# Kernel tuning notes

Measured on AMD Instinct MI355X. Metric: run time of the kernel, lower is better.

Reference implementation:

```python
import jax, jax.numpy as jnp
import numpy as np

N_NODES = 200000
N_EDGES = 800000
N_MOL = 10000
IN_DIM, HDIM, EDGE_DIM = 40, 64, 16
BN_EPS = 1e-5


def _bn_eval(h, gamma, beta, mean, var):
    # BatchNorm1d in eval mode (running stats)
    return gamma * (h - mean) * jax.lax.rsqrt(var + BN_EPS) + beta


def _gine(x, src, dst, edge_attr, We, be, W, b, gamma, beta, mean, var):
    # GINEConv (eps=0): agg_i = sum_{(j->i)} relu(x_j + lin_e(e_ji)); h = nn(x + agg)
    msg = jax.nn.relu(x[src] + edge_attr @ We.T + be)          # [E, d]
    agg = jax.ops.segment_sum(msg, dst, num_segments=x.shape[0])
    h = (x + agg) @ W.T + b                                    # Linear
    h = _bn_eval(h, gamma, beta, mean, var)                    # BatchNorm1d
    return jax.nn.leaky_relu(h)                                # LeakyReLU(0.01); Dropout is identity in eval


def setup_inputs() -> dict:
    key = jax.random.key(0)
    ks = jax.random.split(key, 40)
    d = {}
    d['x'] = jax.random.normal(ks[0], (N_NODES, IN_DIM), jnp.float32)
    d['edge_index'] = jax.random.randint(ks[1], (2, N_EDGES), 0, N_NODES, jnp.int32)
    d['edge_attr'] = jax.random.normal(ks[2], (N_EDGES, EDGE_DIM), jnp.float32)
    d['batch'] = jnp.sort(jax.random.randint(ks[3], (N_NODES,), 0, N_MOL, jnp.int32))
    i = 4
    def nrm(shape, scale=0.05):
        nonlocal i
        i += 1
        return jax.random.normal(ks[i - 1], shape, jnp.float32) * scale
    for l, din in ((1, IN_DIM), (2, HDIM), (3, HDIM)):
        d[f'We{l}'] = nrm((din, EDGE_DIM)); d[f'be{l}'] = nrm((din,))
        d[f'W{l}'] = nrm((HDIM, din)); d[f'b{l}'] = nrm((HDIM,))
        d[f'g{l}'] = jnp.ones((HDIM,), jnp.float32); d[f'bb{l}'] = jnp.zeros((HDIM,), jnp.float32)
        d[f'm{l}'] = nrm((HDIM,)); d[f'v{l}'] = jax.random.uniform(ks[i], (HDIM,), jnp.float32, 0.5, 1.5); i += 1
    D4 = 4 * HDIM
    d['Wl1'] = nrm((D4, D4)); d['bl1'] = nrm((D4,))
    d['Wl2'] = nrm((1, D4)); d['bl2'] = nrm((1,))
    return d


def reference(x, edge_index, edge_attr, batch,
              We1, be1, W1, b1, g1, bb1, m1, v1,
              We2, be2, W2, b2, g2, bb2, m2, v2,
              We3, be3, W3, b3, g3, bb3, m3, v3,
              Wl1, bl1, Wl2, bl2):
    src, dst = edge_index[0], edge_index[1]
    h1 = _gine(x, src, dst, edge_attr, We1, be1, W1, b1, g1, bb1, m1, v1)
    h2 = _gine(h1, src, dst, edge_attr, We2, be2, W2, b2, g2, bb2, m2, v2)
    h3 = _gine(h2, src, dst, edge_attr, We3, be3, W3, b3, g3, bb3, m3, v3)
    h_pool = jax.ops.segment_sum(h3, batch, num_segments=N_MOL)   # global_add_pool
    h_pool_ = h_pool[batch]                                       # repeat_interleave by per-mol counts
    h = jnp.concatenate([h1, h2, h3, h_pool_], axis=1)            # [N, 4*hdim]
    h = jax.nn.leaky_relu(h @ Wl1.T + bl1)
    return h @ Wl2.T + bl2                                        # [N, 1]
```

## Files before the change

kernel.cpp:

```cpp
#include <hip/hip_runtime.h>
#include <hip/hip_bf16.h>

#define N_NODES 200000
#define N_EDGES 800000
#define N_MOL   10000
#define HDIM    64
#define EDGE_DIM 16
#define BN_EPS 1e-5f
#define SCAN_BLOCKS ((N_NODES + 255) / 256)

typedef __attribute__((ext_vector_type(8))) short short8;
typedef __attribute__((ext_vector_type(4))) float f32x4;

__device__ __forceinline__ unsigned int pk2(float a, float b) {
    __hip_bfloat162 h = __float22bfloat162_rn(make_float2(a, b));
    union { __hip_bfloat162 h; unsigned int u; } c;
    c.h = h;
    return c.u;
}
__device__ __forceinline__ short8 cvt8(float4 a, float4 b) {
    union { short8 s; unsigned int u[4]; } r;
    r.u[0] = pk2(a.x, a.y); r.u[1] = pk2(a.z, a.w);
    r.u[2] = pk2(b.x, b.y); r.u[3] = pk2(b.z, b.w);
    return r.s;
}
__device__ __forceinline__ float bf2f(unsigned short u) {
    return __uint_as_float(((unsigned int)u) << 16);
}
__device__ __forceinline__ unsigned short f2bf(float a) {
    union { __hip_bfloat16 h; unsigned short u; } c;
    c.h = __float2bfloat16(a);
    return c.u;
}
__device__ __forceinline__ float4 bf4f(ushort4 u) {
    return make_float4(bf2f(u.x), bf2f(u.y), bf2f(u.z), bf2f(u.w));
}

__global__ __launch_bounds__(256) void cvtx_kernel(
    const float* __restrict__ x, unsigned short* __restrict__ xb)
{
    int i = blockIdx.x * 256 + threadIdx.x;
    if ((size_t)i * 4 >= (size_t)N_NODES * 40) return;
    float4 v = *(const float4*)(x + (size_t)i * 4);
    union { ushort4 s; unsigned int u[2]; } r;
    r.u[0] = pk2(v.x, v.y); r.u[1] = pk2(v.z, v.w);
    *(ushort4*)(xb + (size_t)i * 4) = r.s;
}

__global__ __launch_bounds__(256) void hist_kernel(
    const int* __restrict__ ei, int* __restrict__ counts)
{
    int e = blockIdx.x * 256 + threadIdx.x;
    if (e < N_EDGES) atomicAdd(&counts[ei[N_EDGES + e]], 1);
}

__global__ __launch_bounds__(256) void scan_phase_a(
    const int* __restrict__ counts,
    int* __restrict__ row_ptr, int* __restrict__ block_sums)
{
    __shared__ int lds[256];
    int t = threadIdx.x;
    int i = blockIdx.x * 256 + t;
    int v = (i < N_NODES) ? counts[i] : 0;
    lds[t] = v;
    __syncthreads();
    for (int off = 1; off < 256; off <<= 1) {
        int u = (t >= off) ? lds[t - off] : 0;
        __syncthreads();
        lds[t] += u;
        __syncthreads();
    }
    if (i < N_NODES) row_ptr[i] = lds[t] - v;
    if (t == 255) block_sums[blockIdx.x] = lds[255];
}

__global__ __launch_bounds__(1024) void scan_phase_b(
    int* __restrict__ block_sums)
{
    __shared__ int lds[1024];
    int t = threadIdx.x;
    int v = (t < SCAN_BLOCKS) ? block_sums[t] : 0;
    lds[t] = v;
    __syncthreads();
    for (int off = 1; off < 1024; off <<= 1) {
        int u = (t >= off) ? lds[t - off] : 0;
        __syncthreads();
        lds[t] += u;
        __syncthreads();
    }
    if (t < SCAN_BLOCKS) block_sums[t] = lds[t] - v;
}

__global__ __launch_bounds__(256) void scan_phase_c(
    const int* __restrict__ block_sums,
    int* __restrict__ row_ptr, int* __restrict__ cursor)
{
    int i = blockIdx.x * 256 + threadIdx.x;
    if (i < N_NODES) {
        int v = row_ptr[i] + block_sums[blockIdx.x];
        row_ptr[i] = v;
        cursor[i] = v;
    }
    if (i == 0) row_ptr[N_NODES] = N_EDGES;
}

__global__ __launch_bounds__(256) void scatter_kernel(
    const int* __restrict__ ei, int* __restrict__ cursor,
    int* __restrict__ src_sorted, int* __restrict__ eid_sorted)
{
    int e = blockIdx.x * 256 + threadIdx.x;
    if (e >= N_EDGES) return;
    int d = ei[N_EDGES + e];
    int pos = atomicAdd(&cursor[d], 1);
    src_sorted[pos] = ei[e];
    eid_sorted[pos] = e;
}

#define EMSG_WAVES 8192
template<int DIN>
__global__ __launch_bounds__(256) void emsg_mfma(
    const float* __restrict__ ea,
    const int*   __restrict__ eid_sorted,
    const float* __restrict__ We,
    const float* __restrict__ be,
    unsigned short* __restrict__ emsg)
{
    constexpr int NFT = (DIN + 15) / 16;
    int lane = threadIdx.x & 63;
    int wv = blockIdx.x * 4 + (threadIdx.x >> 6);
    int r = lane & 15, g = lane >> 4;
    const short8 zero8 = (short8){0, 0, 0, 0, 0, 0, 0, 0};

    short8 af[NFT];
    float4 bb[NFT];
    bool   sv[NFT];
#pragma unroll
    for (int ft = 0; ft < NFT; ft++) {
        int feat = ft * 16 + r;
        if (g < 2 && feat < DIN) {
            const float4* w4 = (const float4*)(We + feat * 16 + g * 8);
            af[ft] = cvt8(w4[0], w4[1]);
        } else {
            af[ft] = zero8;
        }
        int feat0 = ft * 16 + g * 4;
        sv[ft] = (feat0 < DIN);
        bb[ft] = sv[ft] ? *(const float4*)(be + feat0)
                        : make_float4(0.f, 0.f, 0.f, 0.f);
    }

    const int NT = N_EDGES / 16;
#pragma unroll 1
    for (int tile = wv; tile < NT; tile += EMSG_WAVES) {
        int j0 = tile * 16;
        int e = eid_sorted[j0 + r];
        short8 zf = zero8;
        if (g < 2) {
            const float4* ep = (const float4*)(ea + (size_t)e * 16 + g * 8);
            zf = cvt8(ep[0], ep[1]);
        }
#pragma unroll
        for (int ft = 0; ft < NFT; ft++) {
            f32x4 acc = (f32x4){0.f, 0.f, 0.f, 0.f};
            acc = __builtin_amdgcn_mfma_f32_16x16x32_bf16(af[ft], zf, acc, 0, 0, 0);
            if (sv[ft]) {
                ushort4 st;
                st.x = f2bf(acc[0] + bb[ft].x);
                st.y = f2bf(acc[1] + bb[ft].y);
                st.z = f2bf(acc[2] + bb[ft].z);
                st.w = f2bf(acc[3] + bb[ft].w);
                *(ushort4*)(emsg + (size_t)(j0 + r) * DIN + ft * 16 + g * 4) = st;
            }
        }
    }
}

template<int DIN>
__global__ __launch_bounds__(256) void agg_pre(
    const unsigned short* __restrict__ feat,
    const int*   __restrict__ row_ptr,
    const int*   __restrict__ src_sorted,
    const unsigned short* __restrict__ emsg,
    unsigned short* __restrict__ AGGb)
{
    int lane = threadIdx.x & 63;
    int wv = blockIdx.x * 4 + (threadIdx.x >> 6);
    int n0 = wv * 8;
    if (n0 >= N_NODES) return;
    int eg = lane >> 4;
    int f4 = lane & 15;
    const bool vf = (f4 * 4 < DIN);
    const int f4c = vf ? f4 : 0;

    int lo = row_ptr[n0];
#pragma unroll 1
    for (int ni = 0; ni < 8; ni++) {
        int node = n0 + ni;
        int hi = row_ptr[node + 1];
        float4 acc = {0.f, 0.f, 0.f, 0.f};
#pragma unroll 1
        for (int j0 = lo; j0 < hi; j0 += 4) {
            int j = j0 + eg;
            bool ev = (j < hi);
            int jc = ev ? j : (hi - 1);
            int s = src_sorted[jc];
            ushort4 xu = *(const ushort4*)(feat + (size_t)s * DIN + f4c * 4);
            ushort4 mu = *(const ushort4*)(emsg + (size_t)jc * DIN + f4c * 4);
            float4 xv = bf4f(xu), mv = bf4f(mu);
            float t0 = fmaxf(xv.x + mv.x, 0.f);
            float t1 = fmaxf(xv.y + mv.y, 0.f);
            float t2 = fmaxf(xv.z + mv.z, 0.f);
            float t3 = fmaxf(xv.w + mv.w, 0.f);
            if (ev && vf) {
                acc.x += t0; acc.y += t1; acc.z += t2; acc.w += t3;
            }
        }
        acc.x += __shfl_xor(acc.x, 16, 64);
        acc.y += __shfl_xor(acc.y, 16, 64);
        acc.z += __shfl_xor(acc.z, 16, 64);
        acc.w += __shfl_xor(acc.w, 16, 64);
        acc.x += __shfl_xor(acc.x, 32, 64);
        acc.y += __shfl_xor(acc.y, 32, 64);
        acc.z += __shfl_xor(acc.z, 32, 64);
        acc.w += __shfl_xor(acc.w, 32, 64);
        if (eg == 0) {
            float4 xd = {0.f, 0.f, 0.f, 0.f};
            if (vf) xd = bf4f(*(const ushort4*)(feat + (size_t)node * DIN + f4 * 4));
            float4 o = vf ? make_float4(acc.x + xd.x, acc.y + xd.y,
                                        acc.z + xd.z, acc.w + xd.w)
                          : make_float4(0.f, 0.f, 0.f, 0.f);
            ushort4 st;
            st.x = f2bf(o.x); st.y = f2bf(o.y);
            st.z = f2bf(o.z); st.w = f2bf(o.w);
            *(ushort4*)(AGGb + (size_t)node * HDIM + f4 * 4) = st;
        }
        lo = hi;
    }
}

template<int DIN>
__global__ __launch_bounds__(256) void agg_kernel(
    const unsigned short* __restrict__ feat,
    const int*   __restrict__ row_ptr,
    const int*   __restrict__ src_sorted,
    const int*   __restrict__ eid_sorted,
    const float* __restrict__ ea,
    const float* __restrict__ We,
    const float* __restrict__ be,
    unsigned short* __restrict__ AGGb)
{
    int lane = threadIdx.x & 63;
    int wv = __builtin_amdgcn_readfirstlane(blockIdx.x * 4 + (threadIdx.x >> 6));
    int n0 = wv * 8;
    if (n0 >= N_NODES) return;
    int f = lane;

    float wrow[16];
    float bias = 0.f;
    if (f < DIN) {
#pragma unroll
        for (int j = 0; j < 16; j++) wrow[j] = We[f * 16 + j];
        bias = be[f];
    } else {
#pragma unroll
        for (int j = 0; j < 16; j++) wrow[j] = 0.f;
    }

    int lo = row_ptr[n0];
    int hi = row_ptr[n0 + 8];
    int cur = 0;
    int nb = row_ptr[n0 + 1];
    float acc = 0.f;

    for (int j0 = lo; j0 < hi; j0 += 8) {
        int jn = min(8, hi - j0);
        int s[8], e[8];
#pragma unroll
        for (int k = 0; k < 8; k++) {
            int j = min(j0 + k, hi - 1);
            s[k] = src_sorted[j];
            e[k] = eid_sorted[j];
        }
        float xv[8];
#pragma unroll
        for (int k = 0; k < 8; k++)
            xv[k] = (f < DIN) ? bf2f(feat[(size_t)s[k] * DIN + f]) : 0.f;

#pragma unroll
        for (int k = 0; k < 8; k++) {
            if (k >= jn) break;
            int j = j0 + k;
            while (j >= nb) {
                float xd = (f < DIN) ? bf2f(feat[(size_t)(n0 + cur) * DIN + f]) : 0.f;
                AGGb[(size_t)(n0 + cur) * HDIM + f] = f2bf(acc + xd);
                acc = 0.f;
                cur++;
                nb = row_ptr[n0 + cur + 1];
            }
            const float4* ep = (const float4*)(ea + (size_t)e[k] * 16);
            float4 q0 = ep[0], q1 = ep[1], q2 = ep[2], q3 = ep[3];
            float a = bias;
            a = fmaf(q0.x, wrow[0],  a); a = fmaf(q0.y, wrow[1],  a);
            a = fmaf(q0.z, wrow[2],  a); a = fmaf(q0.w, wrow[3],  a);
            a = fmaf(q1.x, wrow[4],  a); a = fmaf(q1.y, wrow[5],  a);
            a = fmaf(q1.z, wrow[6],  a); a = fmaf(q1.w, wrow[7],  a);
            a = fmaf(q2.x, wrow[8],  a); a = fmaf(q2.y, wrow[9],  a);
            a = fmaf(q2.z, wrow[10], a); a = fmaf(q2.w, wrow[11], a);
            a = fmaf(q3.x, wrow[12], a); a = fmaf(q3.y, wrow[13], a);
            a = fmaf(q3.z, wrow[14], a); a = fmaf(q3.w, wrow[15], a);
            acc += fmaxf(xv[k] + a, 0.f);
        }
    }
    while (cur < 8) {
        float xd = (f < DIN) ? bf2f(feat[(size_t)(n0 + cur) * DIN + f]) : 0.f;
        AGGb[(size_t)(n0 + cur) * HDIM + f] = f2bf(acc + xd);
        acc = 0.f;
        cur++;
    }
}

template<int DIN>
__global__ __launch_bounds__(256) void node_mfma(
    const unsigned short* __restrict__ AGGb,
    unsigned short* __restrict__ Hb,
    const float* __restrict__ W,
    const float* __restrict__ bias,
    const float* __restrict__ gam,
    const float* __restrict__ bet,
    const float* __restrict__ mean,
    const float* __restrict__ var)
{
    int lane = threadIdx.x & 63;
    int wave = blockIdx.x * 4 + (threadIdx.x >> 6);
    if (wave >= N_NODES / 64) return;
    int n0 = wave * 64;
    int r = lane & 15;
    int g = lane >> 4;

    const short8 zero8 = (short8){0, 0, 0, 0, 0, 0, 0, 0};

    short8 zf[4][2];
#pragma unroll
    for (int nt = 0; nt < 4; nt++) {
        int node = n0 + nt * 16 + r;
        const unsigned short* ar = AGGb + (size_t)node * HDIM;
        zf[nt][0] = *(const short8*)(ar + g * 8);
        zf[nt][1] = *(const short8*)(ar + 32 + g * 8);
    }

    const float4* b4  = (const float4*)bias;
    const float4* g4  = (const float4*)gam;
    const float4* be4 = (const float4*)bet;
    const float4* m4  = (const float4*)mean;
    const float4* v4  = (const float4*)var;

#pragma unroll
    for (int ft = 0; ft < 4; ft++) {
        const float* wr = W + (size_t)(ft * 16 + r) * DIN;
        short8 af[2];
        {
            float4 w0 = *(const float4*)(wr + g * 8);
            float4 w1 = *(const float4*)(wr + g * 8 + 4);
            af[0] = cvt8(w0, w1);
            if (DIN == 64) {
                w0 = *(const float4*)(wr + 32 + g * 8);
                w1 = *(const float4*)(wr + 36 + g * 8);
                af[1] = cvt8(w0, w1);
            } else if (g == 0) {
                w0 = *(const float4*)(wr + 32);
                w1 = *(const float4*)(wr + 36);
                af[1] = cvt8(w0, w1);
            } else {
                af[1] = zero8;
            }
        }

        f32x4 acc[4];
#pragma unroll
        for (int nt = 0; nt < 4; nt++) acc[nt] = (f32x4){0.f, 0.f, 0.f, 0.f};

#pragma unroll
        for (int ks = 0; ks < 2; ks++) {
#pragma unroll
            for (int nt = 0; nt < 4; nt++) {
                acc[nt] = __builtin_amdgcn_mfma_f32_16x16x32_bf16(
                    af[ks], zf[nt][ks], acc[nt], 0, 0, 0);
            }
        }

        int idx = ft * 4 + g;
        float4 bb = b4[idx], gg = g4[idx], bt = be4[idx], mm = m4[idx], vv = v4[idx];
        float s0 = gg.x * rsqrtf(vv.x + BN_EPS);
        float s1 = gg.y * rsqrtf(vv.y + BN_EPS);
        float s2 = gg.z * rsqrtf(vv.z + BN_EPS);
        float s3 = gg.w * rsqrtf(vv.w + BN_EPS);
#pragma unroll
        for (int nt = 0; nt < 4; nt++) {
            int node = n0 + nt * 16 + r;
            float y0 = s0 * (acc[nt][0] + bb.x - mm.x) + bt.x;
            float y1 = s1 * (acc[nt][1] + bb.y - mm.y) + bt.y;
            float y2 = s2 * (acc[nt][2] + bb.z - mm.z) + bt.z;
            float y3 = s3 * (acc[nt][3] + bb.w - mm.w) + bt.w;
            y0 = (y0 > 0.f) ? y0 : 0.01f * y0;
            y1 = (y1 > 0.f) ? y1 : 0.01f * y1;
            y2 = (y2 > 0.f) ? y2 : 0.01f * y2;
            y3 = (y3 > 0.f) ? y3 : 0.01f * y3;
            union { uint2 v; unsigned int u[2]; } st;
            st.u[0] = pk2(y0, y1);
            st.u[1] = pk2(y2, y3);
            *(uint2*)(Hb + (size_t)node * HDIM + ft * 16 + g * 4) = st.v;
        }
    }
}

__global__ __launch_bounds__(256) void pool_kernel(
    const unsigned short* __restrict__ h3b,
    const int*   __restrict__ batch,
    float*       __restrict__ hpool)
{
    int gid = blockIdx.x * 256 + threadIdx.x;
    if (gid >= N_NODES * HDIM) return;
    int i = gid >> 6, f = gid & 63;
    atomicAdd(&hpool[(size_t)batch[i] * HDIM + f], bf2f(h3b[gid]));
}

__global__ __launch_bounds__(256, 2) void head_kernel(
    const unsigned short* __restrict__ h1b,
    const unsigned short* __restrict__ h2b,
    const unsigned short* __restrict__ h3b,
    const float* __restrict__ hpool,
    const int*   __restrict__ batch,
    const float* __restrict__ Wl1, const float* __restrict__ bl1,
    const float* __restrict__ Wl2, const float* __restrict__ bl2,
    float*       __restrict__ out)
{
    __shared__ short8 wlds[4096];

    int tid = threadIdx.x;
    int lane = tid & 63;
    int wave = blockIdx.x * 4 + (tid >> 6);
    bool active = (wave < N_NODES / 64);
    int n0 = active ? wave * 64 : (N_NODES - 64);
    int r = lane & 15;
    int g = lane >> 4;

    short8 zf[4][8];
#pragma unroll
    for (int nt = 0; nt < 4; nt++) {
        int node = n0 + nt * 16 + r;
        const unsigned short* r1 = h1b + (size_t)node * 64;
        const unsigned short* r2 = h2b + (size_t)node * 64;
        const unsigned short* r3 = h3b + (size_t)node * 64;
        const float* rp = hpool + (size_t)batch[node] * 64;
        zf[nt][0] = *(const short8*)(r1 + g * 8);
        zf[nt][1] = *(const short8*)(r1 + 32 + g * 8);
        zf[nt][2] = *(const short8*)(r2 + g * 8);
        zf[nt][3] = *(const short8*)(r2 + 32 + g * 8);
        zf[nt][4] = *(const short8*)(r3 + g * 8);
        zf[nt][5] = *(const short8*)(r3 + 32 + g * 8);
        const float4* q;
        q = (const float4*)(rp + g * 8);        zf[nt][6] = cvt8(q[0], q[1]);
        q = (const float4*)(rp + 32 + g * 8);   zf[nt][7] = cvt8(q[0], q[1]);
    }

    float p[4] = {0.f, 0.f, 0.f, 0.f};
    const float4* bl1_4 = (const float4*)bl1;
    const float4* wl2_4 = (const float4*)Wl2;

#pragma unroll 1
    for (int half = 0; half < 2; half++) {
        if (half) __syncthreads();
#pragma unroll
        for (int i = 0; i < 16; i++) {
            int local = tid + i * 256;
            int ftq = local >> 9;
            int ks  = (local >> 6) & 7;
            int lf  = local & 63;
            int rr = lf & 15, gg = lf >> 4;
            int ft = half * 8 + ftq;
            const float4* q = (const float4*)(Wl1 + (size_t)(ft * 16 + rr) * 256
                                              + ks * 32 + gg * 8);
            wlds[local] = cvt8(q[0], q[1]);
        }
        __syncthreads();

#pragma unroll 1
        for (int ftq = 0; ftq < 8; ftq++) {
            int ft = half * 8 + ftq;
            short8 af[8];
#pragma unroll
            for (int ks = 0; ks < 8; ks++) af[ks] = wlds[(ftq * 8 + ks) * 64 + lane];

            f32x4 acc[4];
#pragma unroll
            for (int nt = 0; nt < 4; nt++) acc[nt] = (f32x4){0.f, 0.f, 0.f, 0.f};
#pragma unroll
            for (int ks = 0; ks < 8; ks++) {
#pragma unroll
                for (int nt = 0; nt < 4; nt++) {
                    acc[nt] = __builtin_amdgcn_mfma_f32_16x16x32_bf16(
                        af[ks], zf[nt][ks], acc[nt], 0, 0, 0);
                }
            }

            float4 bl = bl1_4[ft * 4 + g];
            float4 w2 = wl2_4[ft * 4 + g];
#pragma unroll
            for (int nt = 0; nt < 4; nt++) {
                float a0 = acc[nt][0] + bl.x;
                float a1 = acc[nt][1] + bl.y;
                float a2 = acc[nt][2] + bl.z;
                float a3 = acc[nt][3] + bl.w;
                a0 = (a0 > 0.f) ? a0 : 0.01f * a0;
                a1 = (a1 > 0.f) ? a1 : 0.01f * a1;
                a2 = (a2 > 0.f) ? a2 : 0.01f * a2;
                a3 = (a3 > 0.f) ? a3 : 0.01f * a3;
                p[nt] += w2.x * a0 + w2.y * a1 + w2.z * a2 + w2.w * a3;
            }
        }
    }

    float b2 = bl2[0];
#pragma unroll
    for (int nt = 0; nt < 4; nt++) {
        float s = p[nt];
        s += __shfl_xor(s, 16, 64);
        s += __shfl_xor(s, 32, 64);
        if (g == 0 && active) out[n0 + nt * 16 + r] = s + b2;
    }
}

extern "C" void kernel_launch(void* const* d_in, const int* in_sizes, int n_in,
                              void* d_out, int out_size, void* d_ws, size_t ws_size,
                              hipStream_t stream) {
    const float* x     = (const float*)d_in[0];
    const int*   ei    = (const int*)  d_in[1];
    const float* ea    = (const float*)d_in[2];
    const int*   batch = (const int*)  d_in[3];

    const float* We1 = (const float*)d_in[4];  const float* be1 = (const float*)d_in[5];
    const float* W1  = (const float*)d_in[6];  const float* b1  = (const float*)d_in[7];
    const float* g1  = (const float*)d_in[8];  const float* bb1 = (const float*)d_in[9];
    const float* m1  = (const float*)d_in[10]; const float* v1  = (const float*)d_in[11];

    const float* We2 = (const float*)d_in[12]; const float* be2 = (const float*)d_in[13];
    const float* W2  = (const float*)d_in[14]; const float* b2  = (const float*)d_in[15];
    const float* g2  = (const float*)d_in[16]; const float* bb2 = (const float*)d_in[17];
    const float* m2  = (const float*)d_in[18]; const float* v2  = (const float*)d_in[19];

    const float* We3 = (const float*)d_in[20]; const float* be3 = (const float*)d_in[21];
    const float* W3  = (const float*)d_in[22]; const float* b3  = (const float*)d_in[23];
    const float* g3  = (const float*)d_in[24]; const float* bb3 = (const float*)d_in[25];
    const float* m3  = (const float*)d_in[26]; const float* v3  = (const float*)d_in[27];

    const float* Wl1 = (const float*)d_in[28]; const float* bl1 = (const float*)d_in[29];
    const float* Wl2 = (const float*)d_in[30]; const float* bl2 = (const float*)d_in[31];

    float* out = (float*)d_out;

    char* wp = (char*)d_ws;
    auto carve = [&](size_t bytes) -> char* {
        char* r = wp;
        wp += (bytes + 255) & ~(size_t)255;
        return r;
    };
    unsigned short* AGGb  = (unsigned short*)carve((size_t)N_NODES * HDIM * 2);
    unsigned short* xb    = (unsigned short*)carve((size_t)N_NODES * 40 * 2);
    unsigned short* Hb1   = (unsigned short*)carve((size_t)N_NODES * HDIM * 2);
    unsigned short* Hb2   = (unsigned short*)carve((size_t)N_NODES * HDIM * 2);
    unsigned short* Hb3   = (unsigned short*)carve((size_t)N_NODES * HDIM * 2);
    float* hpool          = (float*)         carve((size_t)N_MOL * HDIM * 4);
    int* counts           = (int*)           carve((size_t)N_NODES * 4);
    int* row_ptr          = (int*)           carve((size_t)(N_NODES + 1) * 4);
    int* cursor           = (int*)           carve((size_t)N_NODES * 4);
    int* src_sorted       = (int*)           carve((size_t)N_EDGES * 4);
    int* eid_sorted       = (int*)           carve((size_t)N_EDGES * 4);
    int* block_sums       = (int*)           carve((size_t)SCAN_BLOCKS * 4);
    unsigned short* emsg  = (unsigned short*)carve((size_t)N_EDGES * HDIM * 2);
    size_t need           = (size_t)(wp - (char*)d_ws);
    bool use_pre = (ws_size >= need);

    hipMemsetAsync(hpool, 0, (size_t)N_MOL * HDIM * sizeof(float), stream);
    hipMemsetAsync(counts, 0, (size_t)N_NODES * sizeof(int), stream);

    dim3 blk(256);
    dim3 cgrid(((size_t)N_NODES * 40 / 4 + 255) / 256);
    dim3 egrid(N_EDGES / 256);
    dim3 mgrid(EMSG_WAVES / 4);
    dim3 sgrid(SCAN_BLOCKS);
    dim3 agrid((N_NODES / 8) / 4);
    dim3 ngrid((N_NODES / 64 + 3) / 4);
    dim3 pgrid((N_NODES * HDIM) / 256);
    dim3 hgrid((N_NODES / 64 + 3) / 4);

    cvtx_kernel<<<cgrid, blk, 0, stream>>>(x, xb);
    hist_kernel<<<egrid, blk, 0, stream>>>(ei, counts);
    scan_phase_a<<<sgrid, blk, 0, stream>>>(counts, row_ptr, block_sums);
    scan_phase_b<<<1, 1024, 0, stream>>>(block_sums);
    scan_phase_c<<<sgrid, blk, 0, stream>>>(block_sums, row_ptr, cursor);
    scatter_kernel<<<egrid, blk, 0, stream>>>(ei, cursor, src_sorted, eid_sorted);

    if (use_pre) {
        emsg_mfma<40><<<mgrid, blk, 0, stream>>>(ea, eid_sorted, We1, be1, emsg);
        agg_pre<40><<<agrid, blk, 0, stream>>>(xb, row_ptr, src_sorted, emsg, AGGb);
        node_mfma<40><<<ngrid, blk, 0, stream>>>(AGGb, Hb1, W1, b1, g1, bb1, m1, v1);
        emsg_mfma<64><<<mgrid, blk, 0, stream>>>(ea, eid_sorted, We2, be2, emsg);
        agg_pre<64><<<agrid, blk, 0, stream>>>(Hb1, row_ptr, src_sorted, emsg, AGGb);
        node_mfma<64><<<ngrid, blk, 0, stream>>>(AGGb, Hb2, W2, b2, g2, bb2, m2, v2);
        emsg_mfma<64><<<mgrid, blk, 0, stream>>>(ea, eid_sorted, We3, be3, emsg);
        agg_pre<64><<<agrid, blk, 0, stream>>>(Hb2, row_ptr, src_sorted, emsg, AGGb);
        node_mfma<64><<<ngrid, blk, 0, stream>>>(AGGb, Hb3, W3, b3, g3, bb3, m3, v3);
    } else {
        agg_kernel<40><<<agrid, blk, 0, stream>>>(xb, row_ptr, src_sorted, eid_sorted,
                                                  ea, We1, be1, AGGb);
        node_mfma<40><<<ngrid, blk, 0, stream>>>(AGGb, Hb1, W1, b1, g1, bb1, m1, v1);
        agg_kernel<64><<<agrid, blk, 0, stream>>>(Hb1, row_ptr, src_sorted, eid_sorted,
                                                  ea, We2, be2, AGGb);
        node_mfma<64><<<ngrid, blk, 0, stream>>>(AGGb, Hb2, W2, b2, g2, bb2, m2, v2);
        agg_kernel<64><<<agrid, blk, 0, stream>>>(Hb2, row_ptr, src_sorted, eid_sorted,
                                                  ea, We3, be3, AGGb);
        node_mfma<64><<<ngrid, blk, 0, stream>>>(AGGb, Hb3, W3, b3, g3, bb3, m3, v3);
    }

    pool_kernel<<<pgrid, blk, 0, stream>>>(Hb3, batch, hpool);
    head_kernel<<<hgrid, blk, 0, stream>>>(Hb1, Hb2, Hb3, hpool, batch,
                                           Wl1, bl1, Wl2, bl2, out);
}
```

Before: 577.4 us.

## Fuse global add pool into last node MFMA kernel and halve head LDS tile

Removes the separate pool_kernel by having the third-layer node_mfma atomically add its fp32 outputs into hpool directly, which saves a re-read of Hb3 and a kernel launch. The pooled sum now uses unrounded fp32 values instead of bf16-rounded ones. Separately, the head kernel stages Wl1 in four passes of 32KB LDS instead of two passes of 64KB, with launch bounds raised to allow more resident blocks, at the cost of extra barriers and reloads.

```diff
diff --git a/kernel.cpp b/kernel.cpp
--- a/kernel.cpp
+++ b/kernel.cpp
@@ -319,7 +319,7 @@
     }
 }
 
-template<int DIN>
+template<int DIN, bool POOL>
 __global__ __launch_bounds__(256) void node_mfma(
     const unsigned short* __restrict__ AGGb,
     unsigned short* __restrict__ Hb,
@@ -328,7 +328,9 @@
     const float* __restrict__ gam,
     const float* __restrict__ bet,
     const float* __restrict__ mean,
-    const float* __restrict__ var)
+    const float* __restrict__ var,
+    const int*   __restrict__ batch,
+    float*       __restrict__ hpool)
 {
     int lane = threadIdx.x & 63;
     int wave = blockIdx.x * 4 + (threadIdx.x >> 6);
@@ -409,22 +411,18 @@
             st.u[0] = pk2(y0, y1);
             st.u[1] = pk2(y2, y3);
             *(uint2*)(Hb + (size_t)node * HDIM + ft * 16 + g * 4) = st.v;
-        }
-    }
-}
-
-__global__ __launch_bounds__(256) void pool_kernel(
-    const unsigned short* __restrict__ h3b,
-    const int*   __restrict__ batch,
-    float*       __restrict__ hpool)
-{
-    int gid = blockIdx.x * 256 + threadIdx.x;
-    if (gid >= N_NODES * HDIM) return;
-    int i = gid >> 6, f = gid & 63;
-    atomicAdd(&hpool[(size_t)batch[i] * HDIM + f], bf2f(h3b[gid]));
-}
-
-__global__ __launch_bounds__(256, 2) void head_kernel(
+            if (POOL) {
+                float* hp = hpool + (size_t)batch[node] * HDIM + ft * 16 + g * 4;
+                atomicAdd(hp + 0, y0);
+                atomicAdd(hp + 1, y1);
+                atomicAdd(hp + 2, y2);
+                atomicAdd(hp + 3, y3);
+            }
+        }
+    }
+}
+
+__global__ __launch_bounds__(256, 4) void head_kernel(
     const unsigned short* __restrict__ h1b,
     const unsigned short* __restrict__ h2b,
     const unsigned short* __restrict__ h3b,
@@ -434,7 +432,7 @@
     const float* __restrict__ Wl2, const float* __restrict__ bl2,
     float*       __restrict__ out)
 {
-    __shared__ short8 wlds[4096];
+    __shared__ short8 wlds[2048];
 
     int tid = threadIdx.x;
     int lane = tid & 63;
@@ -468,16 +466,16 @@
     const float4* wl2_4 = (const float4*)Wl2;
 
 #pragma unroll 1
-    for (int half = 0; half < 2; half++) {
-        if (half) __syncthreads();
-#pragma unroll
-        for (int i = 0; i < 16; i++) {
+    for (int pass = 0; pass < 4; pass++) {
+        if (pass) __syncthreads();
+#pragma unroll
+        for (int i = 0; i < 8; i++) {
             int local = tid + i * 256;
             int ftq = local >> 9;
             int ks  = (local >> 6) & 7;
             int lf  = local & 63;
             int rr = lf & 15, gg = lf >> 4;
-            int ft = half * 8 + ftq;
+            int ft = pass * 4 + ftq;
             const float4* q = (const float4*)(Wl1 + (size_t)(ft * 16 + rr) * 256
                                               + ks * 32 + gg * 8);
             wlds[local] = cvt8(q[0], q[1]);
@@ -485,8 +483,8 @@
         __syncthreads();
 
 #pragma unroll 1
-        for (int ftq = 0; ftq < 8; ftq++) {
-            int ft = half * 8 + ftq;
+        for (int ftq = 0; ftq < 4; ftq++) {
+            int ft = pass * 4 + ftq;
             short8 af[8];
 #pragma unroll
             for (int ks = 0; ks < 8; ks++) af[ks] = wlds[(ftq * 8 + ks) * 64 + lane];
@@ -590,7 +588,6 @@
     dim3 sgrid(SCAN_BLOCKS);
     dim3 agrid((N_NODES / 8) / 4);
     dim3 ngrid((N_NODES / 64 + 3) / 4);
-    dim3 pgrid((N_NODES * HDIM) / 256);
     dim3 hgrid((N_NODES / 64 + 3) / 4);
 
     cvtx_kernel<<<cgrid, blk, 0, stream>>>(x, xb);
@@ -603,26 +600,31 @@
     if (use_pre) {
         emsg_mfma<40><<<mgrid, blk, 0, stream>>>(ea, eid_sorted, We1, be1, emsg);
         agg_pre<40><<<agrid, blk, 0, stream>>>(xb, row_ptr, src_sorted, emsg, AGGb);
-        node_mfma<40><<<ngrid, blk, 0, stream>>>(AGGb, Hb1, W1, b1, g1, bb1, m1, v1);
+        node_mfma<40, false><<<ngrid, blk, 0, stream>>>(AGGb, Hb1, W1, b1, g1, bb1,
+                                                        m1, v1, batch, hpool);
         emsg_mfma<64><<<mgrid, blk, 0, stream>>>(ea, eid_sorted, We2, be2, emsg);
         agg_pre<64><<<agrid, blk, 0, stream>>>(Hb1, row_ptr, src_sorted, emsg, AGGb);
-        node_mfma<64><<<ngrid, blk, 0, stream>>>(AGGb, Hb2, W2, b2, g2, bb2, m2, v2);
+        node_mfma<64, false><<<ngrid, blk, 0, stream>>>(AGGb, Hb2, W2, b2, g2, bb2,
+                                                        m2, v2, batch, hpool);
         emsg_mfma<64><<<mgrid, blk, 0, stream>>>(ea, eid_sorted, We3, be3, emsg);
         agg_pre<64><<<agrid, blk, 0, stream>>>(Hb2, row_ptr, src_sorted, emsg, AGGb);
-        node_mfma<64><<<ngrid, blk, 0, stream>>>(AGGb, Hb3, W3, b3, g3, bb3, m3, v3);
+        node_mfma<64, true><<<ngrid, blk, 0, stream>>>(AGGb, Hb3, W3, b3, g3, bb3,
+                                                       m3, v3, batch, hpool);
     } else {
         agg_kernel<40><<<agrid, blk, 0, stream>>>(xb, row_ptr, src_sorted, eid_sorted,
                                                   ea, We1, be1, AGGb);
-        node_mfma<40><<<ngrid, blk, 0, stream>>>(AGGb, Hb1, W1, b1, g1, bb1, m1, v1);
+        node_mfma<40, false><<<ngrid, blk, 0, stream>>>(AGGb, Hb1, W1, b1, g1, bb1,
+                                                        m1, v1, batch, hpool);
         agg_kernel<64><<<agrid, blk, 0, stream>>>(Hb1, row_ptr, src_sorted, eid_sorted,
                                                   ea, We2, be2, AGGb);
-        node_mfma<64><<<ngrid, blk, 0, stream>>>(AGGb, Hb2, W2, b2, g2, bb2, m2, v2);
+        node_mfma<64, false><<<ngrid, blk, 0, stream>>>(AGGb, Hb2, W2, b2, g2, bb2,
+                                                        m2, v2, batch, hpool);
         agg_kernel<64><<<agrid, blk, 0, stream>>>(Hb2, row_ptr, src_sorted, eid_sorted,
                                                   ea, We3, be3, AGGb);
-        node_mfma<64><<<ngrid, blk, 0, stream>>>(AGGb, Hb3, W3, b3, g3, bb3, m3, v3);
-    }
-
-    pool_kernel<<<pgrid, blk, 0, stream>>>(Hb3, batch, hpool);
+        node_mfma<64, true><<<ngrid, blk, 0, stream>>>(AGGb, Hb3, W3, b3, g3, bb3,
+                                                       m3, v3, batch, hpool);
+    }
+
     head_kernel<<<hgrid, blk, 0, stream>>>(Hb1, Hb2, Hb3, hpool, batch,
                                            Wl1, bl1, Wl2, bl2, out);
 }
```

After: 1.411 ms. +144.3%, slower.
